# Kernel optimization log

Hardware: AMD Instinct MI355X
Metric: run time of the kernel (lower is better)

## Reference

```python
import jax, jax.numpy as jnp
import numpy as np

H = W = 224
NUM_COLS = 1024          # static padded ring width (>= max pixels in any radial ring, ~703)
SHUFFLE_FRACTION = 0.5
BATCH = 128

def _build_maps():
    centre = (H // 2, W // 2)
    Y, X = np.ogrid[:H, :W]
    dist = np.round(np.sqrt((X - centre[0]) ** 2 + (Y - centre[1]) ** 2)).astype(np.int32)
    num_rows = int(dist[0, 0]) + 1
    ax2 = np.zeros_like(dist)
    for d in range(num_rows):
        m = dist == d
        ax2[m] = np.arange(m.sum(), dtype=np.int32)  # row-major order within each ring
    return dist, ax2, num_rows

_DIST_NP, _AX2_NP, NUM_ROWS = _build_maps()
DIST_FLAT = jnp.asarray(_DIST_NP.reshape(-1))  # (H*W,) radial bin of each pixel
AX2_FLAT = jnp.asarray(_AX2_NP.reshape(-1))    # (H*W,) index within its ring

def _process_one(img, mrand, prand):
    # img: (H, W); mrand: (H, W); prand: (NUM_ROWS, NUM_COLS)
    sel = mrand < SHUFFLE_FRACTION
    masked = jnp.where(sel, img, jnp.nan)
    # scatter selected pixels into polar bins (pixel -> (dist, ax2) is a bijection)
    polar = jnp.full((NUM_ROWS, NUM_COLS), jnp.nan, dtype=img.dtype)
    polar = polar.at[DIST_FLAT, AX2_FLAT].set(masked.reshape(-1))
    # random per-row permutation of columns
    perm = jnp.argsort(prand, axis=1)
    shuf = jnp.take_along_axis(polar, perm, axis=1)
    # compact the non-NaN shuffled values (in column order) back into the
    # originally-occupied columns (in ascending order) -- same as the TF
    # argsort(dists)/boolean-mask scatter, expressed with static shapes.
    src_order = jnp.argsort(jnp.isnan(shuf), axis=1)    # stable: non-NaN cols first
    vals = jnp.take_along_axis(shuf, src_order, axis=1)
    dst_order = jnp.argsort(jnp.isnan(polar), axis=1)   # stable: occupied cols first
    rows = jnp.arange(NUM_ROWS)[:, None]
    reinserted = shuf.at[rows, dst_order].set(vals)
    # gather each pixel's (possibly shuffled) value and write back selected pixels
    new_vals = reinserted[DIST_FLAT, AX2_FLAT].reshape(H, W)
    return jnp.where(sel, new_vals, img)

def setup_inputs() -> dict:
    key = jax.random.key(0)
    k1, k2, k3 = jax.random.split(key, 3)
    images = jax.random.normal(k1, (BATCH, H, W, 1), dtype=jnp.float32)
    mask_rand = jax.random.uniform(k2, (BATCH, H, W), dtype=jnp.float32)
    perm_rand = jax.random.uniform(k3, (BATCH, NUM_ROWS, NUM_COLS), dtype=jnp.float32)
    return {"images": images, "mask_rand": mask_rand, "perm_rand": perm_rand}

def reference(images, mask_rand, perm_rand):
    out = jax.vmap(_process_one)(images[..., 0], mask_rand, perm_rand)
    return out[..., None]
```

## Files before the change

kernel.cpp:

```cpp
#include <hip/hip_runtime.h>

#define IMG_H 224
#define IMG_W 224
#define HW (IMG_H * IMG_W)
#define HWB (HW / 8)
#define NUM_ROWS 159
#define NUM_COLS 1024
#define BATCH 128
#define OVF_CAP 4096
#define MAXC 11
#define NBUCK 512
#define NHWORDS (NBUCK / 2)
#define WPL (NHWORDS / 64)

__device__ __forceinline__ int isqrt_i(int v) {
    int u = (int)sqrtf((float)v);
    while (u > 0 && u * u > v) --u;
    while ((u + 1) * (u + 1) <= v) ++u;
    return u;
}

__device__ __forceinline__ void lds_fence() {
    asm volatile("s_waitcnt lgkmcnt(0)" ::: "memory");
}

__global__ __launch_bounds__(256) void pre_pass(
    const float4* __restrict__ img4, const float4* __restrict__ mask4,
    float4* __restrict__ out4, unsigned char* __restrict__ selb,
    unsigned short* __restrict__ ring_pix, int* __restrict__ ring_cnt,
    int* __restrict__ ovf_cnt) {
    const int bid = blockIdx.x;
    const int tid = threadIdx.x;
    __shared__ int scnt[256];

    if (bid < NUM_ROWS) {
        const int d = bid;
        if (d == 0 && tid == 0) ovf_cnt[0] = 0;
        int cnt = 0;
        int x0l = 0, x1l = -1, x0r = 0, x1r = -1;
        if (tid < IMG_H) {
            const int dy = tid - 112;
            const int Araw = (d == 0) ? 0 : (d * d - d + 1);
            int A = Araw - dy * dy;
            if (A < 0) A = 0;
            const int B = d * d + d - dy * dy;
            if (B >= 0) {
                const int hi = isqrt_i(B);
                int lo = isqrt_i(A);
                if (lo * lo < A) ++lo;
                if (lo <= hi) {
                    if (lo == 0) {
                        x0l = 112 - min(hi, 112);
                        x1l = 112 + min(hi, 111);
                    } else {
                        x0l = 112 - min(hi, 112);
                        x1l = 112 - lo;
                        x0r = 112 + lo;
                        x1r = 112 + min(hi, 111);
                    }
                    cnt = max(0, x1l - x0l + 1) + max(0, x1r - x0r + 1);
                }
            }
        }
        scnt[tid] = cnt;
        __syncthreads();
        for (int off = 1; off < 256; off <<= 1) {
            const int mine = scnt[tid];
            const int add = (tid >= off) ? scnt[tid - off] : 0;
            __syncthreads();
            scnt[tid] = mine + add;
            __syncthreads();
        }
        if (tid < IMG_H && cnt > 0) {
            int j = d * NUM_COLS + (scnt[tid] - cnt);
            const int rowbase = tid * IMG_W;
            for (int x = x0l; x <= x1l; ++x) ring_pix[j++] = (unsigned short)(rowbase + x);
            for (int x = x0r; x <= x1r; ++x) ring_pix[j++] = (unsigned short)(rowbase + x);
        }
        if (tid == 255) ring_cnt[d] = scnt[255];
    } else {
        const int t = (bid - NUM_ROWS) * 256 + tid;
        const float4 i0 = img4[2 * t];
        const float4 i1 = img4[2 * t + 1];
        const float4 m0 = mask4[2 * t];
        const float4 m1 = mask4[2 * t + 1];
        out4[2 * t] = i0;
        out4[2 * t + 1] = i1;
        const unsigned by = (m0.x < 0.5f ? 1u : 0u) | (m0.y < 0.5f ? 2u : 0u) |
                            (m0.z < 0.5f ? 4u : 0u) | (m0.w < 0.5f ? 8u : 0u) |
                            (m1.x < 0.5f ? 16u : 0u) | (m1.y < 0.5f ? 32u : 0u) |
                            (m1.z < 0.5f ? 64u : 0u) | (m1.w < 0.5f ? 128u : 0u);
        selb[t] = (unsigned char)by;
    }
}

__device__ __forceinline__ void sort_run(unsigned long long* __restrict__ srt,
                                         int s, int e) {
    for (int i = s + 1; i < e; ++i) {
        const unsigned long long key = srt[i];
        int q = i - 1;
        while (q >= s && srt[q] > key) {
            srt[q + 1] = srt[q];
            --q;
        }
        srt[q + 1] = key;
    }
}

template <int CAP>
__device__ int gather_count_sort(
    int b, int d, int lane, int n,
    const float* __restrict__ img, const unsigned char* __restrict__ selb,
    const float* __restrict__ prand, float* __restrict__ out,
    const unsigned short* __restrict__ ring_pix,
    unsigned long long* __restrict__ srt, unsigned* __restrict__ hist,
    float* __restrict__ vlds) {
    const float* imgb = img + (size_t)b * HW;
    const unsigned char* sbb = selb + (size_t)b * HWB;
    const float* prb = prand + ((size_t)b * NUM_ROWS + d) * NUM_COLS;
    float* outb = out + (size_t)b * HW;
    const unsigned long long ltmask = (1ull << lane) - 1ull;
    const unsigned short* rp = ring_pix + d * NUM_COLS;

#pragma unroll
    for (int t = 0; t < WPL; ++t) hist[t * 64 + lane] = 0;

    int p[MAXC];
    unsigned char sb[MAXC];
    unsigned kb[MAXC];
#pragma unroll
    for (int c = 0; c < MAXC; ++c)
        if (c * 64 < n) p[c] = rp[min(c * 64 + lane, n - 1)];
#pragma unroll
    for (int c = 0; c < MAXC; ++c)
        if (c * 64 < n) sb[c] = sbb[p[c] >> 3];
#pragma unroll
    for (int c = 0; c < MAXC; ++c)
        if (c * 64 < n) kb[c] = __float_as_uint(prb[c * 64 + lane]);

    unsigned selm = 0;
#pragma unroll
    for (int c = 0; c < MAXC; ++c)
        if (c * 64 < n) {
            if ((c * 64 + lane) < n && ((sb[c] >> (p[c] & 7)) & 1)) selm |= 1u << c;
        }

    float v[MAXC];
#pragma unroll
    for (int c = 0; c < MAXC; ++c)
        if (c * 64 < n) {
            if ((selm >> c) & 1) v[c] = imgb[p[c]];
        }

    lds_fence();

    int jc[MAXC], oldc[MAXC];
    int base = 0;
#pragma unroll
    for (int c = 0; c < MAXC; ++c)
        if (c * 64 < n) {
            const bool sel = (selm >> c) & 1;
            const unsigned long long ball = __ballot(sel);
            if (sel) {
                jc[c] = base + __popcll(ball & ltmask);
                const int bk = (int)(__uint_as_float(kb[c]) * (float)NBUCK);
                const unsigned sh = (unsigned)((bk & 1) * 16);
                const unsigned old = atomicAdd(&hist[bk >> 1], 1u << sh);
                oldc[c] = (int)((old >> sh) & 0xffffu);
            }
            base += __popcll(ball);
        }
    const int k = base;
    if (k > CAP) return k;
    if (k == 0) return 0;

    lds_fence();

    unsigned cw[WPL], stw[WPL];
    unsigned run = 0;
#pragma unroll
    for (int t = 0; t < WPL; ++t) {
        const unsigned w = hist[lane * WPL + t];
        cw[t] = w;
        const unsigned c0 = w & 0xffffu;
        stw[t] = run | ((run + c0) << 16);
        run += c0 + (w >> 16);
    }
    const unsigned own = run;
#pragma unroll
    for (int off = 1; off < 64; off <<= 1) {
        const unsigned o = __shfl_up(run, off, 64);
        if (lane >= off) run += o;
    }
    const unsigned bx = run - own;
    const unsigned bxp = bx | (bx << 16);
#pragma unroll
    for (int t = 0; t < WPL; ++t) {
        stw[t] += bxp;
        hist[lane * WPL + t] = stw[t];
    }

    lds_fence();

#pragma unroll
    for (int c = 0; c < MAXC; ++c)
        if (c * 64 < n) {
            if ((selm >> c) & 1) {
                const int bk = (int)(__uint_as_float(kb[c]) * (float)NBUCK);
                const unsigned sh = (unsigned)((bk & 1) * 16);
                const int pos = (int)((hist[bk >> 1] >> sh) & 0xffffu) + oldc[c];
                srt[pos] = ((unsigned long long)kb[c] << 16) | (unsigned)jc[c];
                vlds[jc[c]] = v[c];
            }
        }

    lds_fence();

    bool any2 = false;
#pragma unroll
    for (int t = 0; t < WPL; ++t)
        if ((cw[t] & 0xffffu) >= 2 || (cw[t] >> 16) >= 2) any2 = true;
    if (__ballot(any2) != 0ull) {
#pragma unroll
        for (int t = 0; t < WPL; ++t) {
            const unsigned s0 = stw[t] & 0xffffu, c0 = cw[t] & 0xffffu;
            const unsigned s1 = stw[t] >> 16, c1 = cw[t] >> 16;
            if (c0 >= 2) sort_run(srt, (int)s0, (int)(s0 + c0));
            if (c1 >= 2) sort_run(srt, (int)s1, (int)(s1 + c1));
        }
        lds_fence();
    }

    const unsigned short* s16 = (const unsigned short*)srt;
#pragma unroll
    for (int c = 0; c < MAXC; ++c)
        if (c * 64 < n) {
            if ((selm >> c) & 1) {
                const int jp = s16[4 * jc[c]];
                outb[p[c]] = vlds[jp];
            }
        }
    return k;
}

template <int CAP>
__device__ int gather_count_sort_dyn(
    int b, int d, int lane, int n,
    const float* __restrict__ img, const unsigned char* __restrict__ selb,
    const float* __restrict__ prand, float* __restrict__ out,
    const unsigned short* __restrict__ ring_pix,
    unsigned long long* __restrict__ srt, unsigned* __restrict__ hist,
    float* __restrict__ vlds) {
    const float* imgb = img + (size_t)b * HW;
    const unsigned char* sbb = selb + (size_t)b * HWB;
    const float* prb = prand + ((size_t)b * NUM_ROWS + d) * NUM_COLS;
    float* outb = out + (size_t)b * HW;
    const unsigned long long ltmask = (1ull << lane) - 1ull;
    const unsigned short* rp = ring_pix + d * NUM_COLS;

    for (int t = 0; t < WPL; ++t) hist[t * 64 + lane] = 0;
    lds_fence();

    int base = 0;
    for (int c0 = 0; c0 < n; c0 += 64) {
        const int i = c0 + lane;
        bool sel = false;
        int pp = 0;
        unsigned kk = 0;
        if (i < n) {
            pp = rp[i];
            kk = __float_as_uint(prb[min(i, NUM_COLS - 1)]);
            sel = (sbb[pp >> 3] >> (pp & 7)) & 1;
        }
        const unsigned long long ball = __ballot(sel);
        if (sel) {
            const int j = base + __popcll(ball & ltmask);
            if (j < CAP) vlds[j] = imgb[pp];
            const int bk = (int)(__uint_as_float(kk) * (float)NBUCK);
            atomicAdd(&hist[bk >> 1], 1u << ((bk & 1) * 16));
        }
        base += __popcll(ball);
    }
    const int k = base;
    if (k > CAP) return k;
    if (k == 0) return 0;
    lds_fence();

    unsigned neww[WPL];
    unsigned run = 0;
    for (int t = 0; t < WPL; ++t) {
        const unsigned w = hist[lane * WPL + t];
        const unsigned c0 = w & 0xffffu;
        neww[t] = run | ((run + c0) << 16);
        run += c0 + (w >> 16);
    }
    const unsigned own = run;
    for (int off = 1; off < 64; off <<= 1) {
        const unsigned o = __shfl_up(run, off, 64);
        if (lane >= off) run += o;
    }
    const unsigned bx = run - own;
    const unsigned bxp = bx | (bx << 16);
    unsigned st[WPL];
    for (int t = 0; t < WPL; ++t) {
        st[t] = neww[t] + bxp;
        hist[lane * WPL + t] = st[t];
    }
    lds_fence();

    int jb = 0;
    for (int c0 = 0; c0 < n; c0 += 64) {
        const int i = c0 + lane;
        bool sel = false;
        unsigned kk = 0;
        if (i < n) {
            const int pp = rp[i];
            kk = __float_as_uint(prb[min(i, NUM_COLS - 1)]);
            sel = (sbb[pp >> 3] >> (pp & 7)) & 1;
        }
        const unsigned long long ball = __ballot(sel);
        if (sel) {
            const int j = jb + __popcll(ball & ltmask);
            const int bk = (int)(__uint_as_float(kk) * (float)NBUCK);
            const unsigned sh = (unsigned)((bk & 1) * 16);
            const unsigned old = atomicAdd(&hist[bk >> 1], 1u << sh);
            const int pos = (int)((old >> sh) & 0xffffu);
            srt[pos] = ((unsigned long long)kk << 16) | (unsigned)j;
        }
        jb += __popcll(ball);
    }
    lds_fence();

    for (int t = 0; t < WPL; ++t) {
        const unsigned wend = hist[lane * WPL + t];
        const unsigned ws0 = st[t];
        sort_run(srt, (int)(ws0 & 0xffffu), (int)(wend & 0xffffu));
        sort_run(srt, (int)(ws0 >> 16), (int)(wend >> 16));
    }
    lds_fence();

    const unsigned short* s16 = (const unsigned short*)srt;
    jb = 0;
    for (int c0 = 0; c0 < n; c0 += 64) {
        const int i = c0 + lane;
        bool sel = false;
        int pp = 0;
        if (i < n) {
            pp = rp[i];
            sel = (sbb[pp >> 3] >> (pp & 7)) & 1;
        }
        const unsigned long long ball = __ballot(sel);
        if (sel) {
            const int j = jb + __popcll(ball & ltmask);
            const int jp = s16[4 * j];
            outb[pp] = vlds[jp];
        }
        jb += __popcll(ball);
    }
    return k;
}

__global__ __launch_bounds__(256, 5) void radial_shuffle(
    const float* __restrict__ img, const unsigned char* __restrict__ selb,
    const float* __restrict__ prand, float* __restrict__ out,
    const unsigned short* __restrict__ ring_pix, const int* __restrict__ ring_cnt,
    int* __restrict__ ovf_cnt, int* __restrict__ ovf_list) {
    const int tid = threadIdx.x;
    const int wid = tid >> 6;
    const int lane = tid & 63;
    const int xcd = blockIdx.x & 7;
    const int g = (blockIdx.x >> 3) * 4 + wid;
    const int b = xcd * (BATCH / 8) + g / NUM_ROWS;
    const int d = g % NUM_ROWS;
    const int n = __builtin_amdgcn_readfirstlane(ring_cnt[d]);

    __shared__ unsigned long long srt_s[4][512];
    __shared__ unsigned hist_s[4][NHWORDS];
    __shared__ float vl_s[4][512];

    int k;
    if (n <= MAXC * 64) {
        k = gather_count_sort<512>(b, d, lane, n, img, selb, prand, out,
                                   ring_pix, srt_s[wid], hist_s[wid], vl_s[wid]);
    } else {
        k = gather_count_sort_dyn<512>(b, d, lane, n, img, selb, prand, out,
                                       ring_pix, srt_s[wid], hist_s[wid],
                                       vl_s[wid]);
    }

    if (k > 512) {
        if (lane == 0) {
            const int idx = atomicAdd(ovf_cnt, 1);
            if (idx < OVF_CAP) ovf_list[idx] = b * NUM_ROWS + d;
        }
    }
}

__global__ __launch_bounds__(64) void overflow_sort(
    const float* __restrict__ img, const unsigned char* __restrict__ selb,
    const float* __restrict__ prand, float* __restrict__ out,
    const unsigned short* __restrict__ ring_pix, const int* __restrict__ ring_cnt,
    const int* __restrict__ ovf_cnt, const int* __restrict__ ovf_list) {
    __shared__ unsigned long long srt[1024];
    __shared__ unsigned hist[NHWORDS];
    __shared__ float vlds[1024];
    const int m = min(*ovf_cnt, OVF_CAP);
    const int lane = threadIdx.x;
    for (int t = blockIdx.x; t < m; t += gridDim.x) {
        const int bd = ovf_list[t];
        const int b = bd / NUM_ROWS;
        const int d = bd % NUM_ROWS;
        const int n = __builtin_amdgcn_readfirstlane(ring_cnt[d]);
        if (n <= MAXC * 64) {
            gather_count_sort<1024>(b, d, lane, n, img, selb, prand, out,
                                    ring_pix, srt, hist, vlds);
        } else {
            gather_count_sort_dyn<1024>(b, d, lane, n, img, selb, prand, out,
                                        ring_pix, srt, hist, vlds);
        }
        __syncthreads();
    }
}

extern "C" void kernel_launch(void* const* d_in, const int* in_sizes, int n_in,
                              void* d_out, int out_size, void* d_ws, size_t ws_size,
                              hipStream_t stream) {
    const float* img   = (const float*)d_in[0];
    const float* mask  = (const float*)d_in[1];
    const float* prand = (const float*)d_in[2];
    float* out = (float*)d_out;

    unsigned short* ring_pix = (unsigned short*)d_ws;
    int* ring_cnt = (int*)((char*)d_ws + NUM_ROWS * NUM_COLS * sizeof(unsigned short));
    int* ovf_cnt  = ring_cnt + NUM_ROWS;
    int* ovf_list = ovf_cnt + 1;
    unsigned char* selb = (unsigned char*)(ovf_list + OVF_CAP);

    hipLaunchKernelGGL(pre_pass, dim3(NUM_ROWS + BATCH * HW / 8 / 256), dim3(256),
                       0, stream, (const float4*)img, (const float4*)mask,
                       (float4*)out, selb, ring_pix, ring_cnt, ovf_cnt);
    hipLaunchKernelGGL(radial_shuffle, dim3(BATCH * NUM_ROWS / 4), dim3(256), 0,
                       stream, img, selb, prand, out, ring_pix, ring_cnt,
                       ovf_cnt, ovf_list);
    hipLaunchKernelGGL(overflow_sort, dim3(16), dim3(64), 0, stream,
                       img, selb, prand, out, ring_pix, ring_cnt,
                       ovf_cnt, ovf_list);
}
```

Before: 206.8 us.

## Split sort records into key/index/value arrays and drop LDS fences

Replaces the packed 64-bit key|index sort records and the separate value buffer with struct-of-arrays LDS storage (32-bit key, 16-bit index, float value). Values move with their keys during the scatter and insertion sort, so the final write reads the value directly instead of doing a dependent index-then-value lookup. Bucket offsets now come from a second atomicAdd pass rather than stored per-element old counts. Several lds_fence waits are removed, and the launch-bounds occupancy hint rises from 5 to 6 to use the smaller LDS footprint. Dropping the explicit waitcnt fences relies on the compiler ordering same-wave LDS accesses, which is a correctness risk.

Result: no change. 208.7 us (+0.9%).

```diff
diff --git a/kernel.cpp b/kernel.cpp
--- a/kernel.cpp
+++ b/kernel.cpp
@@ -94,16 +94,41 @@
     }
 }
 
-__device__ __forceinline__ void sort_run(unsigned long long* __restrict__ srt,
-                                         int s, int e) {
+__device__ __forceinline__ void sort_run3(unsigned* __restrict__ k32,
+                                          unsigned short* __restrict__ j16,
+                                          float* __restrict__ val,
+                                          int s, int e) {
     for (int i = s + 1; i < e; ++i) {
-        const unsigned long long key = srt[i];
+        const unsigned key = k32[i];
+        const unsigned short jj = j16[i];
+        const float vv = val[i];
         int q = i - 1;
-        while (q >= s && srt[q] > key) {
-            srt[q + 1] = srt[q];
+        while (q >= s && (k32[q] > key || (k32[q] == key && j16[q] > jj))) {
+            k32[q + 1] = k32[q];
+            j16[q + 1] = j16[q];
+            val[q + 1] = val[q];
             --q;
         }
-        srt[q + 1] = key;
+        k32[q + 1] = key;
+        j16[q + 1] = jj;
+        val[q + 1] = vv;
+    }
+}
+
+__device__ __forceinline__ void sort_run2(unsigned* __restrict__ k32,
+                                          unsigned short* __restrict__ j16,
+                                          int s, int e) {
+    for (int i = s + 1; i < e; ++i) {
+        const unsigned key = k32[i];
+        const unsigned short jj = j16[i];
+        int q = i - 1;
+        while (q >= s && (k32[q] > key || (k32[q] == key && j16[q] > jj))) {
+            k32[q + 1] = k32[q];
+            j16[q + 1] = j16[q];
+            --q;
+        }
+        k32[q + 1] = key;
+        j16[q + 1] = jj;
     }
 }
 
@@ -113,8 +138,8 @@
     const float* __restrict__ img, const unsigned char* __restrict__ selb,
     const float* __restrict__ prand, float* __restrict__ out,
     const unsigned short* __restrict__ ring_pix,
-    unsigned long long* __restrict__ srt, unsigned* __restrict__ hist,
-    float* __restrict__ vlds) {
+    unsigned* __restrict__ srtk, unsigned short* __restrict__ srtj,
+    float* __restrict__ srtv, unsigned* __restrict__ hist) {
     const float* imgb = img + (size_t)b * HW;
     const unsigned char* sbb = selb + (size_t)b * HWB;
     const float* prb = prand + ((size_t)b * NUM_ROWS + d) * NUM_COLS;
@@ -152,9 +177,7 @@
             if ((selm >> c) & 1) v[c] = imgb[p[c]];
         }
 
-    lds_fence();
-
-    int jc[MAXC], oldc[MAXC];
+    int jc[MAXC];
     int base = 0;
 #pragma unroll
     for (int c = 0; c < MAXC; ++c)
@@ -164,17 +187,13 @@
             if (sel) {
                 jc[c] = base + __popcll(ball & ltmask);
                 const int bk = (int)(__uint_as_float(kb[c]) * (float)NBUCK);
-                const unsigned sh = (unsigned)((bk & 1) * 16);
-                const unsigned old = atomicAdd(&hist[bk >> 1], 1u << sh);
-                oldc[c] = (int)((old >> sh) & 0xffffu);
+                atomicAdd(&hist[bk >> 1], 1u << ((bk & 1) * 16));
             }
             base += __popcll(ball);
         }
     const int k = base;
     if (k > CAP) return k;
     if (k == 0) return 0;
-
-    lds_fence();
 
     unsigned cw[WPL], stw[WPL];
     unsigned run = 0;
@@ -200,21 +219,19 @@
         hist[lane * WPL + t] = stw[t];
     }
 
-    lds_fence();
-
 #pragma unroll
     for (int c = 0; c < MAXC; ++c)
         if (c * 64 < n) {
             if ((selm >> c) & 1) {
                 const int bk = (int)(__uint_as_float(kb[c]) * (float)NBUCK);
                 const unsigned sh = (unsigned)((bk & 1) * 16);
-                const int pos = (int)((hist[bk >> 1] >> sh) & 0xffffu) + oldc[c];
-                srt[pos] = ((unsigned long long)kb[c] << 16) | (unsigned)jc[c];
-                vlds[jc[c]] = v[c];
+                const unsigned old = atomicAdd(&hist[bk >> 1], 1u << sh);
+                const int pos = (int)((old >> sh) & 0xffffu);
+                srtk[pos] = kb[c];
+                srtj[pos] = (unsigned short)jc[c];
+                srtv[pos] = v[c];
             }
         }
-
-    lds_fence();
 
     bool any2 = false;
 #pragma unroll
@@ -225,20 +242,15 @@
         for (int t = 0; t < WPL; ++t) {
             const unsigned s0 = stw[t] & 0xffffu, c0 = cw[t] & 0xffffu;
             const unsigned s1 = stw[t] >> 16, c1 = cw[t] >> 16;
-            if (c0 >= 2) sort_run(srt, (int)s0, (int)(s0 + c0));
-            if (c1 >= 2) sort_run(srt, (int)s1, (int)(s1 + c1));
-        }
-        lds_fence();
-    }
-
-    const unsigned short* s16 = (const unsigned short*)srt;
+            if (c0 >= 2) sort_run3(srtk, srtj, srtv, (int)s0, (int)(s0 + c0));
+            if (c1 >= 2) sort_run3(srtk, srtj, srtv, (int)s1, (int)(s1 + c1));
+        }
+    }
+
 #pragma unroll
     for (int c = 0; c < MAXC; ++c)
         if (c * 64 < n) {
-            if ((selm >> c) & 1) {
-                const int jp = s16[4 * jc[c]];
-                outb[p[c]] = vlds[jp];
-            }
+            if ((selm >> c) & 1) outb[p[c]] = srtv[jc[c]];
         }
     return k;
 }
@@ -249,14 +261,15 @@
     const float* __restrict__ img, const unsigned char* __restrict__ selb,
     const float* __restrict__ prand, float* __restrict__ out,
     const unsigned short* __restrict__ ring_pix,
-    unsigned long long* __restrict__ srt, unsigned* __restrict__ hist,
-    float* __restrict__ vlds) {
+    unsigned* __restrict__ srtk, unsigned short* __restrict__ srtj,
+    float* __restrict__ srtv, unsigned* __restrict__ hist) {
     const float* imgb = img + (size_t)b * HW;
     const unsigned char* sbb = selb + (size_t)b * HWB;
     const float* prb = prand + ((size_t)b * NUM_ROWS + d) * NUM_COLS;
     float* outb = out + (size_t)b * HW;
     const unsigned long long ltmask = (1ull << lane) - 1ull;
     const unsigned short* rp = ring_pix + d * NUM_COLS;
+    unsigned* pixmap = (unsigned*)srtv;
 
     for (int t = 0; t < WPL; ++t) hist[t * 64 + lane] = 0;
     lds_fence();
@@ -275,7 +288,7 @@
         const unsigned long long ball = __ballot(sel);
         if (sel) {
             const int j = base + __popcll(ball & ltmask);
-            if (j < CAP) vlds[j] = imgb[pp];
+            if (j < CAP) pixmap[j] = (unsigned)pp;
             const int bk = (int)(__uint_as_float(kk) * (float)NBUCK);
             atomicAdd(&hist[bk >> 1], 1u << ((bk & 1) * 16));
         }
@@ -325,7 +338,8 @@
             const unsigned sh = (unsigned)((bk & 1) * 16);
             const unsigned old = atomicAdd(&hist[bk >> 1], 1u << sh);
             const int pos = (int)((old >> sh) & 0xffffu);
-            srt[pos] = ((unsigned long long)kk << 16) | (unsigned)j;
+            srtk[pos] = kk;
+            srtj[pos] = (unsigned short)j;
         }
         jb += __popcll(ball);
     }
@@ -334,12 +348,11 @@
     for (int t = 0; t < WPL; ++t) {
         const unsigned wend = hist[lane * WPL + t];
         const unsigned ws0 = st[t];
-        sort_run(srt, (int)(ws0 & 0xffffu), (int)(wend & 0xffffu));
-        sort_run(srt, (int)(ws0 >> 16), (int)(wend >> 16));
+        sort_run2(srtk, srtj, (int)(ws0 & 0xffffu), (int)(wend & 0xffffu));
+        sort_run2(srtk, srtj, (int)(ws0 >> 16), (int)(wend >> 16));
     }
     lds_fence();
 
-    const unsigned short* s16 = (const unsigned short*)srt;
     jb = 0;
     for (int c0 = 0; c0 < n; c0 += 64) {
         const int i = c0 + lane;
@@ -351,16 +364,16 @@
         }
         const unsigned long long ball = __ballot(sel);
         if (sel) {
-            const int j = jb + __popcll(ball & ltmask);
-            const int jp = s16[4 * j];
-            outb[pp] = vlds[jp];
+            const int q = jb + __popcll(ball & ltmask);
+            const int jp = srtj[q];
+            outb[pp] = imgb[pixmap[jp]];
         }
         jb += __popcll(ball);
     }
     return k;
 }
 
-__global__ __launch_bounds__(256, 5) void radial_shuffle(
+__global__ __launch_bounds__(256, 6) void radial_shuffle(
     const float* __restrict__ img, const unsigned char* __restrict__ selb,
     const float* __restrict__ prand, float* __restrict__ out,
     const unsigned short* __restrict__ ring_pix, const int* __restrict__ ring_cnt,
@@ -374,18 +387,20 @@
     const int d = g % NUM_ROWS;
     const int n = __builtin_amdgcn_readfirstlane(ring_cnt[d]);
 
-    __shared__ unsigned long long srt_s[4][512];
+    __shared__ unsigned srtk_s[4][512];
+    __shared__ unsigned short srtj_s[4][512];
+    __shared__ float srtv_s[4][512];
     __shared__ unsigned hist_s[4][NHWORDS];
-    __shared__ float vl_s[4][512];
 
     int k;
     if (n <= MAXC * 64) {
         k = gather_count_sort<512>(b, d, lane, n, img, selb, prand, out,
-                                   ring_pix, srt_s[wid], hist_s[wid], vl_s[wid]);
+                                   ring_pix, srtk_s[wid], srtj_s[wid],
+                                   srtv_s[wid], hist_s[wid]);
     } else {
         k = gather_count_sort_dyn<512>(b, d, lane, n, img, selb, prand, out,
-                                       ring_pix, srt_s[wid], hist_s[wid],
-                                       vl_s[wid]);
+                                       ring_pix, srtk_s[wid], srtj_s[wid],
+                                       srtv_s[wid], hist_s[wid]);
     }
 
     if (k > 512) {
@@ -401,9 +416,10 @@
     const float* __restrict__ prand, float* __restrict__ out,
     const unsigned short* __restrict__ ring_pix, const int* __restrict__ ring_cnt,
     const int* __restrict__ ovf_cnt, const int* __restrict__ ovf_list) {
-    __shared__ unsigned long long srt[1024];
+    __shared__ unsigned srtk[1024];
+    __shared__ unsigned short srtj[1024];
+    __shared__ float srtv[1024];
     __shared__ unsigned hist[NHWORDS];
-    __shared__ float vlds[1024];
     const int m = min(*ovf_cnt, OVF_CAP);
     const int lane = threadIdx.x;
     for (int t = blockIdx.x; t < m; t += gridDim.x) {
@@ -413,10 +429,10 @@
         const int n = __builtin_amdgcn_readfirstlane(ring_cnt[d]);
         if (n <= MAXC * 64) {
             gather_count_sort<1024>(b, d, lane, n, img, selb, prand, out,
-                                    ring_pix, srt, hist, vlds);
+                                    ring_pix, srtk, srtj, srtv, hist);
         } else {
             gather_count_sort_dyn<1024>(b, d, lane, n, img, selb, prand, out,
-                                        ring_pix, srt, hist, vlds);
+                                        ring_pix, srtk, srtj, srtv, hist);
         }
         __syncthreads();
     }
```

## Sort pixel indices instead of value slots to shrink LDS and raise occupancy

Applied to the files above, without the earlier changes.

The counting-sort entries now hold a 32-bit key plus a 16-bit source pixel index in split arrays. This replaces the packed 64-bit key/slot word and drops the per-wave staging buffer for image values. Outputs are gathered straight from global memory with the sorted pixel index. Bucket positions come from a second atomic pass instead of saving per-element offsets, which frees registers, and launch bounds rise from 5 to 8 blocks per CU. In exchange, the final image reads become scattered global gathers, and the insertion-sort pass over buckets now always runs instead of being skipped when no bucket has two or more entries.

Measured after the change: 211.8 us. 2.4% more time.

```diff
diff --git a/kernel.cpp b/kernel.cpp
--- a/kernel.cpp
+++ b/kernel.cpp
@@ -94,16 +94,20 @@
     }
 }
 
-__device__ __forceinline__ void sort_run(unsigned long long* __restrict__ srt,
-                                         int s, int e) {
+__device__ __forceinline__ void sort_run2(unsigned* __restrict__ k32,
+                                          unsigned short* __restrict__ p16,
+                                          int s, int e) {
     for (int i = s + 1; i < e; ++i) {
-        const unsigned long long key = srt[i];
+        const unsigned key = k32[i];
+        const unsigned short pp = p16[i];
         int q = i - 1;
-        while (q >= s && srt[q] > key) {
-            srt[q + 1] = srt[q];
+        while (q >= s && (k32[q] > key || (k32[q] == key && p16[q] > pp))) {
+            k32[q + 1] = k32[q];
+            p16[q + 1] = p16[q];
             --q;
         }
-        srt[q + 1] = key;
+        k32[q + 1] = key;
+        p16[q + 1] = pp;
     }
 }
 
@@ -113,8 +117,8 @@
     const float* __restrict__ img, const unsigned char* __restrict__ selb,
     const float* __restrict__ prand, float* __restrict__ out,
     const unsigned short* __restrict__ ring_pix,
-    unsigned long long* __restrict__ srt, unsigned* __restrict__ hist,
-    float* __restrict__ vlds) {
+    unsigned* __restrict__ srtk, unsigned short* __restrict__ srtp,
+    unsigned* __restrict__ hist) {
     const float* imgb = img + (size_t)b * HW;
     const unsigned char* sbb = selb + (size_t)b * HWB;
     const float* prb = prand + ((size_t)b * NUM_ROWS + d) * NUM_COLS;
@@ -145,16 +149,9 @@
             if ((c * 64 + lane) < n && ((sb[c] >> (p[c] & 7)) & 1)) selm |= 1u << c;
         }
 
-    float v[MAXC];
-#pragma unroll
-    for (int c = 0; c < MAXC; ++c)
-        if (c * 64 < n) {
-            if ((selm >> c) & 1) v[c] = imgb[p[c]];
-        }
-
-    lds_fence();
-
-    int jc[MAXC], oldc[MAXC];
+    lds_fence();
+
+    int jc[MAXC];
     int base = 0;
 #pragma unroll
     for (int c = 0; c < MAXC; ++c)
@@ -164,9 +161,7 @@
             if (sel) {
                 jc[c] = base + __popcll(ball & ltmask);
                 const int bk = (int)(__uint_as_float(kb[c]) * (float)NBUCK);
-                const unsigned sh = (unsigned)((bk & 1) * 16);
-                const unsigned old = atomicAdd(&hist[bk >> 1], 1u << sh);
-                oldc[c] = (int)((old >> sh) & 0xffffu);
+                atomicAdd(&hist[bk >> 1], 1u << ((bk & 1) * 16));
             }
             base += __popcll(ball);
         }
@@ -176,14 +171,13 @@
 
     lds_fence();
 
-    unsigned cw[WPL], stw[WPL];
+    unsigned neww[WPL];
     unsigned run = 0;
 #pragma unroll
     for (int t = 0; t < WPL; ++t) {
         const unsigned w = hist[lane * WPL + t];
-        cw[t] = w;
         const unsigned c0 = w & 0xffffu;
-        stw[t] = run | ((run + c0) << 16);
+        neww[t] = run | ((run + c0) << 16);
         run += c0 + (w >> 16);
     }
     const unsigned own = run;
@@ -194,10 +188,11 @@
     }
     const unsigned bx = run - own;
     const unsigned bxp = bx | (bx << 16);
-#pragma unroll
-    for (int t = 0; t < WPL; ++t) {
-        stw[t] += bxp;
-        hist[lane * WPL + t] = stw[t];
+    unsigned st[WPL];
+#pragma unroll
+    for (int t = 0; t < WPL; ++t) {
+        st[t] = neww[t] + bxp;
+        hist[lane * WPL + t] = st[t];
     }
 
     lds_fence();
@@ -208,36 +203,31 @@
             if ((selm >> c) & 1) {
                 const int bk = (int)(__uint_as_float(kb[c]) * (float)NBUCK);
                 const unsigned sh = (unsigned)((bk & 1) * 16);
-                const int pos = (int)((hist[bk >> 1] >> sh) & 0xffffu) + oldc[c];
-                srt[pos] = ((unsigned long long)kb[c] << 16) | (unsigned)jc[c];
-                vlds[jc[c]] = v[c];
+                const unsigned old = atomicAdd(&hist[bk >> 1], 1u << sh);
+                const int pos = (int)((old >> sh) & 0xffffu);
+                srtk[pos] = kb[c];
+                srtp[pos] = (unsigned short)p[c];
             }
         }
 
     lds_fence();
 
-    bool any2 = false;
-#pragma unroll
-    for (int t = 0; t < WPL; ++t)
-        if ((cw[t] & 0xffffu) >= 2 || (cw[t] >> 16) >= 2) any2 = true;
-    if (__ballot(any2) != 0ull) {
-#pragma unroll
-        for (int t = 0; t < WPL; ++t) {
-            const unsigned s0 = stw[t] & 0xffffu, c0 = cw[t] & 0xffffu;
-            const unsigned s1 = stw[t] >> 16, c1 = cw[t] >> 16;
-            if (c0 >= 2) sort_run(srt, (int)s0, (int)(s0 + c0));
-            if (c1 >= 2) sort_run(srt, (int)s1, (int)(s1 + c1));
-        }
-        lds_fence();
-    }
-
-    const unsigned short* s16 = (const unsigned short*)srt;
+#pragma unroll
+    for (int t = 0; t < WPL; ++t) {
+        const unsigned wend = hist[lane * WPL + t];
+        const unsigned ws0 = st[t];
+        sort_run2(srtk, srtp, (int)(ws0 & 0xffffu), (int)(wend & 0xffffu));
+        sort_run2(srtk, srtp, (int)(ws0 >> 16), (int)(wend >> 16));
+    }
+
+    lds_fence();
+
 #pragma unroll
     for (int c = 0; c < MAXC; ++c)
         if (c * 64 < n) {
             if ((selm >> c) & 1) {
-                const int jp = s16[4 * jc[c]];
-                outb[p[c]] = vlds[jp];
+                const int psrc = srtp[jc[c]];
+                outb[p[c]] = imgb[psrc];
             }
         }
     return k;
@@ -249,8 +239,8 @@
     const float* __restrict__ img, const unsigned char* __restrict__ selb,
     const float* __restrict__ prand, float* __restrict__ out,
     const unsigned short* __restrict__ ring_pix,
-    unsigned long long* __restrict__ srt, unsigned* __restrict__ hist,
-    float* __restrict__ vlds) {
+    unsigned* __restrict__ srtk, unsigned short* __restrict__ srtp,
+    unsigned* __restrict__ hist) {
     const float* imgb = img + (size_t)b * HW;
     const unsigned char* sbb = selb + (size_t)b * HWB;
     const float* prb = prand + ((size_t)b * NUM_ROWS + d) * NUM_COLS;
@@ -262,6 +252,49 @@
     lds_fence();
 
     int base = 0;
+    for (int c0 = 0; c0 < n; c0 += 64) {
+        const int i = c0 + lane;
+        bool sel = false;
+        unsigned kk = 0;
+        if (i < n) {
+            const int pp = rp[i];
+            kk = __float_as_uint(prb[min(i, NUM_COLS - 1)]);
+            sel = (sbb[pp >> 3] >> (pp & 7)) & 1;
+        }
+        const unsigned long long ball = __ballot(sel);
+        if (sel) {
+            const int bk = (int)(__uint_as_float(kk) * (float)NBUCK);
+            atomicAdd(&hist[bk >> 1], 1u << ((bk & 1) * 16));
+        }
+        base += __popcll(ball);
+    }
+    const int k = base;
+    if (k > CAP) return k;
+    if (k == 0) return 0;
+    lds_fence();
+
+    unsigned neww[WPL];
+    unsigned run = 0;
+    for (int t = 0; t < WPL; ++t) {
+        const unsigned w = hist[lane * WPL + t];
+        const unsigned c0 = w & 0xffffu;
+        neww[t] = run | ((run + c0) << 16);
+        run += c0 + (w >> 16);
+    }
+    const unsigned own = run;
+    for (int off = 1; off < 64; off <<= 1) {
+        const unsigned o = __shfl_up(run, off, 64);
+        if (lane >= off) run += o;
+    }
+    const unsigned bx = run - own;
+    const unsigned bxp = bx | (bx << 16);
+    unsigned st[WPL];
+    for (int t = 0; t < WPL; ++t) {
+        st[t] = neww[t] + bxp;
+        hist[lane * WPL + t] = st[t];
+    }
+    lds_fence();
+
     for (int c0 = 0; c0 < n; c0 += 64) {
         const int i = c0 + lane;
         bool sel = false;
@@ -272,75 +305,26 @@
             kk = __float_as_uint(prb[min(i, NUM_COLS - 1)]);
             sel = (sbb[pp >> 3] >> (pp & 7)) & 1;
         }
-        const unsigned long long ball = __ballot(sel);
         if (sel) {
-            const int j = base + __popcll(ball & ltmask);
-            if (j < CAP) vlds[j] = imgb[pp];
-            const int bk = (int)(__uint_as_float(kk) * (float)NBUCK);
-            atomicAdd(&hist[bk >> 1], 1u << ((bk & 1) * 16));
-        }
-        base += __popcll(ball);
-    }
-    const int k = base;
-    if (k > CAP) return k;
-    if (k == 0) return 0;
-    lds_fence();
-
-    unsigned neww[WPL];
-    unsigned run = 0;
-    for (int t = 0; t < WPL; ++t) {
-        const unsigned w = hist[lane * WPL + t];
-        const unsigned c0 = w & 0xffffu;
-        neww[t] = run | ((run + c0) << 16);
-        run += c0 + (w >> 16);
-    }
-    const unsigned own = run;
-    for (int off = 1; off < 64; off <<= 1) {
-        const unsigned o = __shfl_up(run, off, 64);
-        if (lane >= off) run += o;
-    }
-    const unsigned bx = run - own;
-    const unsigned bxp = bx | (bx << 16);
-    unsigned st[WPL];
-    for (int t = 0; t < WPL; ++t) {
-        st[t] = neww[t] + bxp;
-        hist[lane * WPL + t] = st[t];
-    }
-    lds_fence();
-
-    int jb = 0;
-    for (int c0 = 0; c0 < n; c0 += 64) {
-        const int i = c0 + lane;
-        bool sel = false;
-        unsigned kk = 0;
-        if (i < n) {
-            const int pp = rp[i];
-            kk = __float_as_uint(prb[min(i, NUM_COLS - 1)]);
-            sel = (sbb[pp >> 3] >> (pp & 7)) & 1;
-        }
-        const unsigned long long ball = __ballot(sel);
-        if (sel) {
-            const int j = jb + __popcll(ball & ltmask);
             const int bk = (int)(__uint_as_float(kk) * (float)NBUCK);
             const unsigned sh = (unsigned)((bk & 1) * 16);
             const unsigned old = atomicAdd(&hist[bk >> 1], 1u << sh);
             const int pos = (int)((old >> sh) & 0xffffu);
-            srt[pos] = ((unsigned long long)kk << 16) | (unsigned)j;
-        }
-        jb += __popcll(ball);
+            srtk[pos] = kk;
+            srtp[pos] = (unsigned short)pp;
+        }
     }
     lds_fence();
 
     for (int t = 0; t < WPL; ++t) {
         const unsigned wend = hist[lane * WPL + t];
         const unsigned ws0 = st[t];
-        sort_run(srt, (int)(ws0 & 0xffffu), (int)(wend & 0xffffu));
-        sort_run(srt, (int)(ws0 >> 16), (int)(wend >> 16));
-    }
-    lds_fence();
-
-    const unsigned short* s16 = (const unsigned short*)srt;
-    jb = 0;
+        sort_run2(srtk, srtp, (int)(ws0 & 0xffffu), (int)(wend & 0xffffu));
+        sort_run2(srtk, srtp, (int)(ws0 >> 16), (int)(wend >> 16));
+    }
+    lds_fence();
+
+    int jb = 0;
     for (int c0 = 0; c0 < n; c0 += 64) {
         const int i = c0 + lane;
         bool sel = false;
@@ -351,16 +335,15 @@
         }
         const unsigned long long ball = __ballot(sel);
         if (sel) {
-            const int j = jb + __popcll(ball & ltmask);
-            const int jp = s16[4 * j];
-            outb[pp] = vlds[jp];
+            const int q = jb + __popcll(ball & ltmask);
+            outb[pp] = imgb[srtp[q]];
         }
         jb += __popcll(ball);
     }
     return k;
 }
 
-__global__ __launch_bounds__(256, 5) void radial_shuffle(
+__global__ __launch_bounds__(256, 8) void radial_shuffle(
     const float* __restrict__ img, const unsigned char* __restrict__ selb,
     const float* __restrict__ prand, float* __restrict__ out,
     const unsigned short* __restrict__ ring_pix, const int* __restrict__ ring_cnt,
@@ -374,18 +357,19 @@
     const int d = g % NUM_ROWS;
     const int n = __builtin_amdgcn_readfirstlane(ring_cnt[d]);
 
-    __shared__ unsigned long long srt_s[4][512];
+    __shared__ unsigned srtk_s[4][512];
+    __shared__ unsigned short srtp_s[4][512];
     __shared__ unsigned hist_s[4][NHWORDS];
-    __shared__ float vl_s[4][512];
 
     int k;
     if (n <= MAXC * 64) {
         k = gather_count_sort<512>(b, d, lane, n, img, selb, prand, out,
-                                   ring_pix, srt_s[wid], hist_s[wid], vl_s[wid]);
+                                   ring_pix, srtk_s[wid], srtp_s[wid],
+                                   hist_s[wid]);
     } else {
         k = gather_count_sort_dyn<512>(b, d, lane, n, img, selb, prand, out,
-                                       ring_pix, srt_s[wid], hist_s[wid],
-                                       vl_s[wid]);
+                                       ring_pix, srtk_s[wid], srtp_s[wid],
+                                       hist_s[wid]);
     }
 
     if (k > 512) {
@@ -401,9 +385,9 @@
     const float* __restrict__ prand, float* __restrict__ out,
     const unsigned short* __restrict__ ring_pix, const int* __restrict__ ring_cnt,
     const int* __restrict__ ovf_cnt, const int* __restrict__ ovf_list) {
-    __shared__ unsigned long long srt[1024];
+    __shared__ unsigned srtk[1024];
+    __shared__ unsigned short srtp[1024];
     __shared__ unsigned hist[NHWORDS];
-    __shared__ float vlds[1024];
     const int m = min(*ovf_cnt, OVF_CAP);
     const int lane = threadIdx.x;
     for (int t = blockIdx.x; t < m; t += gridDim.x) {
@@ -413,10 +397,10 @@
         const int n = __builtin_amdgcn_readfirstlane(ring_cnt[d]);
         if (n <= MAXC * 64) {
             gather_count_sort<1024>(b, d, lane, n, img, selb, prand, out,
-                                    ring_pix, srt, hist, vlds);
+                                    ring_pix, srtk, srtp, hist);
         } else {
             gather_count_sort_dyn<1024>(b, d, lane, n, img, selb, prand, out,
-                                        ring_pix, srt, hist, vlds);
+                                        ring_pix, srtk, srtp, hist);
         }
         __syncthreads();
     }
```
